# Performance work log

Hardware: AMD Instinct MI355X
Metric: run time of the kernel (lower is better)

The kernel has to match this reference:

```python
import jax, jax.numpy as jnp
import numpy as np

B, T, IN, H, OUT = 64, 512, 512, 1024, 512


def setup_inputs() -> dict:
    key = jax.random.key(0)
    ks = jax.random.split(key, 12)
    s = 0.05
    return {
        "x": jax.random.normal(ks[0], (B, T, IN), dtype=jnp.float32),
        "W_ih0": jax.random.normal(ks[1], (H, IN), dtype=jnp.float32) * s,
        "W_hh0": jax.random.normal(ks[2], (H, H), dtype=jnp.float32) * s,
        "b_ih0": jax.random.normal(ks[3], (H,), dtype=jnp.float32) * s,
        "b_hh0": jax.random.normal(ks[4], (H,), dtype=jnp.float32) * s,
        "W_ih1": jax.random.normal(ks[5], (H, H), dtype=jnp.float32) * s,
        "W_hh1": jax.random.normal(ks[6], (H, H), dtype=jnp.float32) * s,
        "b_ih1": jax.random.normal(ks[7], (H,), dtype=jnp.float32) * s,
        "b_hh1": jax.random.normal(ks[8], (H,), dtype=jnp.float32) * s,
        "fc_w": jax.random.normal(ks[9], (OUT, H), dtype=jnp.float32) * s,
        "fc_b": jax.random.normal(ks[10], (OUT,), dtype=jnp.float32) * s,
    }


def reference(x, W_ih0, W_hh0, b_ih0, b_hh0, W_ih1, W_hh1, b_ih1, b_hh1, fc_w, fc_b):
    # Two-layer Elman RNN with tanh, scanned over time.
    batch = x.shape[0]
    hid = W_hh0.shape[0]
    h_init = jnp.zeros((2, batch, hid), dtype=x.dtype)

    def step(h, x_t):
        h0 = jnp.tanh(x_t @ W_ih0.T + b_ih0 + h[0] @ W_hh0.T + b_hh0)
        h1 = jnp.tanh(h0 @ W_ih1.T + b_ih1 + h[1] @ W_hh1.T + b_hh1)
        return jnp.stack([h0, h1]), h1

    h_final, ys = jax.lax.scan(step, h_init, jnp.swapaxes(x, 0, 1))  # ys: [T,B,H]
    outputs = jnp.swapaxes(ys, 0, 1)  # [B,T,H]
    # Note: the torch module computes fc(outputs[:, -1, :]) but discards it;
    # the returned values are (outputs, h) only.
    return (outputs, h_final)
```

## Files before the change

kernel.cpp:

```cpp
#include <hip/hip_runtime.h>
#include <math.h>

#define RNN_B 64
#define RNN_T 512
#define RNN_IN 512
#define RNN_H 1024


__device__ __forceinline__ void fma16(float4 acc[4], const float4 w, const float4 h) {
  acc[0].x = fmaf(w.x, h.x, acc[0].x); acc[0].y = fmaf(w.x, h.y, acc[0].y);
  acc[0].z = fmaf(w.x, h.z, acc[0].z); acc[0].w = fmaf(w.x, h.w, acc[0].w);
  acc[1].x = fmaf(w.y, h.x, acc[1].x); acc[1].y = fmaf(w.y, h.y, acc[1].y);
  acc[1].z = fmaf(w.y, h.z, acc[1].z); acc[1].w = fmaf(w.y, h.w, acc[1].w);
  acc[2].x = fmaf(w.z, h.x, acc[2].x); acc[2].y = fmaf(w.z, h.y, acc[2].y);
  acc[2].z = fmaf(w.z, h.z, acc[2].z); acc[2].w = fmaf(w.z, h.w, acc[2].w);
  acc[3].x = fmaf(w.w, h.x, acc[3].x); acc[3].y = fmaf(w.w, h.y, acc[3].y);
  acc[3].z = fmaf(w.w, h.z, acc[3].z); acc[3].w = fmaf(w.w, h.w, acc[3].w);
}

__device__ __forceinline__ void reduce4(float4 acc[4]) {
  #pragma unroll
  for (int m = 8; m <= 16; m <<= 1) {
    #pragma unroll
    for (int c = 0; c < 4; ++c) {
      acc[c].x += __shfl_xor(acc[c].x, m, 64);
      acc[c].y += __shfl_xor(acc[c].y, m, 64);
      acc[c].z += __shfl_xor(acc[c].z, m, 64);
      acc[c].w += __shfl_xor(acc[c].w, m, 64);
    }
  }
}

__device__ __forceinline__ void grid_barrier(unsigned* flags, unsigned* gen,
                                             unsigned target) {
  __syncthreads();
  const int tid = threadIdx.x;
  const int bid = blockIdx.x;
  if (tid == 0)
    __hip_atomic_store(flags + bid, target, __ATOMIC_RELAXED,
                       __HIP_MEMORY_SCOPE_AGENT);
  if (bid == 0) {
    if (tid < 64) {
      for (;;) {
        bool ok = true;
        #pragma unroll
        for (int i = 0; i < 4; ++i) {
          unsigned v = __hip_atomic_load(flags + tid + 64 * i, __ATOMIC_RELAXED,
                                         __HIP_MEMORY_SCOPE_AGENT);
          ok &= (v >= target);
        }
        if (__all(ok)) break;
        __builtin_amdgcn_s_sleep(1);
      }
      if (tid < 8)
        __hip_atomic_store(gen + tid * 16, target, __ATOMIC_RELAXED,
                           __HIP_MEMORY_SCOPE_AGENT);
    }
  } else if (tid == 0) {
    while (__hip_atomic_load(gen + (bid & 7) * 16, __ATOMIC_RELAXED,
                             __HIP_MEMORY_SCOPE_AGENT) < target) {
      __builtin_amdgcn_s_sleep(2);
    }
  }
  if (tid == 0)
    __builtin_amdgcn_fence(__ATOMIC_ACQUIRE, "agent");
  __syncthreads();
}

__global__ __launch_bounds__(256) void pre_kernel(
    const float* __restrict__ x, const float* __restrict__ Wih0,
    const float* __restrict__ bih0, const float* __restrict__ bhh0,
    float* __restrict__ out)
{
  __shared__ float xs[64][68];
  __shared__ float wl[64][68];
  const int t  = blockIdx.y;
  const int n0 = blockIdx.x * 64;
  const int tid = threadIdx.x;
  const int tx = tid & 15;
  const int ty = tid >> 4;
  const int kf4 = tid & 15;
  const int row = tid >> 4;

  float4 acc[4];
  acc[0] = acc[1] = acc[2] = acc[3] = make_float4(0.f, 0.f, 0.f, 0.f);

  for (int k0 = 0; k0 < RNN_IN; k0 += 64) {
    #pragma unroll
    for (int r = 0; r < 4; ++r) {
      const int rr = row + 16 * r;
      float4 v = *(const float4*)(x + ((size_t)rr * RNN_T + t) * RNN_IN + k0 + kf4 * 4);
      xs[kf4*4+0][rr] = v.x; xs[kf4*4+1][rr] = v.y;
      xs[kf4*4+2][rr] = v.z; xs[kf4*4+3][rr] = v.w;
      float4 w = *(const float4*)(Wih0 + (size_t)(n0 + rr) * RNN_IN + k0 + kf4 * 4);
      wl[kf4*4+0][rr] = w.x; wl[kf4*4+1][rr] = w.y;
      wl[kf4*4+2][rr] = w.z; wl[kf4*4+3][rr] = w.w;
    }
    __syncthreads();
    #pragma unroll 8
    for (int k = 0; k < 64; ++k) {
      float4 xv = *(const float4*)&xs[k][tx * 4];
      float4 wv = *(const float4*)&wl[k][ty * 4];
      fma16(acc, wv, xv);
    }
    __syncthreads();
  }

  #pragma unroll
  for (int i = 0; i < 4; ++i) {
    const int n = n0 + ty * 4 + i;
    const float bi = bih0[n] + bhh0[n];
    xs[ty*4+i][tx*4+0] = acc[i].x + bi;
    xs[ty*4+i][tx*4+1] = acc[i].y + bi;
    xs[ty*4+i][tx*4+2] = acc[i].z + bi;
    xs[ty*4+i][tx*4+3] = acc[i].w + bi;
  }
  __syncthreads();
  #pragma unroll
  for (int rep = 0; rep < 4; ++rep) {
    const int idx = tid + 256 * rep;
    const int nloc = idx >> 4;
    const int bq4 = idx & 15;
    float4 o = *(const float4*)(&xs[nloc][bq4 * 4]);
    const int gbid = ((n0 + nloc) >> 3) * 2 + (bq4 >> 3);
    const int off  = (nloc & 7) * 32 + (bq4 & 7) * 4;
    const size_t dst = ((size_t)(gbid >> 2) * RNN_T + t) * RNN_H
                     + (size_t)(gbid & 3) * 256 + off;
    *(float4*)(out + dst) = o;
  }
}

__global__ __launch_bounds__(1024) void rnn_kernel(
    const float* __restrict__ Whh0, const float* __restrict__ Wih1,
    const float* __restrict__ Whh1, const float* __restrict__ bih1,
    const float* __restrict__ bhh1, float* __restrict__ out,
    float* __restrict__ hws)
{
  __shared__ float w0[RNN_H * 8];
  __shared__ float w1[RNN_H * 16];
  __shared__ float part0[16 * 256];
  __shared__ float part1[16 * 256];
  __shared__ float tile[256];

  const int tid = threadIdx.x;
  const int bid = blockIdx.x;
  const int n0 = (bid >> 1) * 8;
  const int b0 = (bid & 1) * 32;

  for (int i = tid; i < 8 * RNN_H; i += 1024) {
    const int nl = i >> 10, k = i & 1023;
    w0[k * 8 + nl]             = Whh0[(size_t)(n0 + nl) * RNN_H + k];
    w1[k * 8 + nl]             = Wih1[(size_t)(n0 + nl) * RNN_H + k];
    w1[8 * RNN_H + k * 8 + nl] = Whh1[(size_t)(n0 + nl) * RNN_H + k];
  }
  float mybias = 0.f;
  if (tid < 256) mybias = bih1[n0 + (tid >> 5)] + bhh1[n0 + (tid >> 5)];
  __syncthreads();

  const int wav  = tid >> 6;
  const int lane = tid & 63;
  const int nh   = lane >> 5;
  const int kq   = (lane >> 3) & 3;
  const int bq   = lane & 7;
  const int kbase = wav * 4 + kq;
  const int hoff = kbase * RNN_B + b0 + bq * 4;
  const int woff = kbase * 8 + nh * 4;

  unsigned* flags = (unsigned*)(hws + 262144);
  unsigned* gen   = (unsigned*)(hws + 262400);
  float* h0buf[2] = { hws,         hws + 131072 };
  float* h1buf[2] = { hws + 65536, hws + 196608 };
  const int houtoff = (n0 + (tid >> 5)) * RNN_B + b0 + (tid & 31);

  float preval = 0.f, nextpre = 0.f;
  if (tid < 256)
    preval = out[(size_t)(bid >> 2) * RNN_T * RNN_H + (size_t)(bid & 3) * 256 + tid];

  for (int p = 0; p <= RNN_T; ++p) {
    if (tid < 256 && p + 1 < RNN_T)
      nextpre = out[((size_t)(bid >> 2) * RNN_T + (p + 1)) * RNN_H
                    + (size_t)(bid & 3) * 256 + tid];
    if (p < RNN_T) {
      const float* hp = h0buf[(p + 1) & 1] + hoff;
      const float* wp = w0 + woff;
      float4 acc[4];
      acc[0] = acc[1] = acc[2] = acc[3] = make_float4(0.f, 0.f, 0.f, 0.f);
      #pragma unroll
      for (int j = 0; j < 16; ++j) {
        float4 hv = *(const float4*)(hp + j * 64 * RNN_B);
        float4 wv = *(const float4*)(wp + j * 64 * 8);
        fma16(acc, wv, hv);
      }
      reduce4(acc);
      if ((lane & 24) == 0) {
        #pragma unroll
        for (int c = 0; c < 4; ++c)
          *(float4*)(part0 + wav * 256 + (nh * 4 + c) * 32 + bq * 4) = acc[c];
      }
    }
    if (p >= 1) {
      const int t = p - 1;
      const float* h0t = h0buf[t & 1]       + hoff;
      const float* h1p = h1buf[(t + 1) & 1] + hoff;
      const float* wpa = w1 + woff;
      const float* wpb = w1 + 8 * RNN_H + woff;
      float4 acc[4];
      acc[0] = acc[1] = acc[2] = acc[3] = make_float4(0.f, 0.f, 0.f, 0.f);
      #pragma unroll
      for (int j = 0; j < 16; ++j) {
        float4 hv0 = *(const float4*)(h0t + j * 64 * RNN_B);
        float4 wv0 = *(const float4*)(wpa + j * 64 * 8);
        float4 hv1 = *(const float4*)(h1p + j * 64 * RNN_B);
        float4 wv1 = *(const float4*)(wpb + j * 64 * 8);
        fma16(acc, wv0, hv0);
        fma16(acc, wv1, hv1);
      }
      reduce4(acc);
      if ((lane & 24) == 0) {
        #pragma unroll
        for (int c = 0; c < 4; ++c)
          *(float4*)(part1 + wav * 256 + (nh * 4 + c) * 32 + bq * 4) = acc[c];
      }
    }
    __syncthreads();
    if (tid < 256) {
      if (p < RNN_T) {
        float s = preval;
        #pragma unroll
        for (int w = 0; w < 16; ++w) s += part0[w * 256 + tid];
        __hip_atomic_store(&h0buf[p & 1][houtoff], tanhf(s), __ATOMIC_RELAXED,
                           __HIP_MEMORY_SCOPE_AGENT);
      }
      if (p >= 1) {
        float s = mybias;
        #pragma unroll
        for (int w = 0; w < 16; ++w) s += part1[w * 256 + tid];
        float v = tanhf(s);
        __hip_atomic_store(&h1buf[(p - 1) & 1][houtoff], v, __ATOMIC_RELAXED,
                           __HIP_MEMORY_SCOPE_AGENT);
        tile[tid] = v;
      }
      preval = nextpre;
    }
    __syncthreads();
    if (p >= 1 && tid < 64) {
      const int b = tid >> 1, half = tid & 1;
      float4 o;
      o.x = tile[(half * 4 + 0) * 32 + b];
      o.y = tile[(half * 4 + 1) * 32 + b];
      o.z = tile[(half * 4 + 2) * 32 + b];
      o.w = tile[(half * 4 + 3) * 32 + b];
      *(float4*)(out + ((size_t)(b0 + b) * RNN_T + (p - 1)) * RNN_H + n0 + half * 4) = o;
    }
    if (p < RNN_T) grid_barrier(flags, gen, (unsigned)(p + 1));
  }

  if (tid < 512) {
    const int l   = tid >> 8;
    const int idx = tid & 255;
    const int nl  = idx >> 5, bl = idx & 31;
    const float* hf = (l == 0) ? (hws + 131072) : (hws + 196608);
    float v = __hip_atomic_load(hf + (size_t)(n0 + nl) * RNN_B + b0 + bl,
                                __ATOMIC_RELAXED, __HIP_MEMORY_SCOPE_AGENT);
    out[(size_t)RNN_B * RNN_T * RNN_H + ((size_t)l * RNN_B + b0 + bl) * RNN_H + n0 + nl]
        = v;
  }
}

extern "C" void kernel_launch(void* const* d_in, const int* in_sizes, int n_in,
                              void* d_out, int out_size, void* d_ws, size_t ws_size,
                              hipStream_t stream) {
  (void)in_sizes; (void)n_in; (void)out_size; (void)ws_size;
  const float* x    = (const float*)d_in[0];
  const float* Wih0 = (const float*)d_in[1];
  const float* Whh0 = (const float*)d_in[2];
  const float* bih0 = (const float*)d_in[3];
  const float* bhh0 = (const float*)d_in[4];
  const float* Wih1 = (const float*)d_in[5];
  const float* Whh1 = (const float*)d_in[6];
  const float* bih1 = (const float*)d_in[7];
  const float* bhh1 = (const float*)d_in[8];
  float* out = (float*)d_out;
  float* hws = (float*)d_ws;

  hipMemsetAsync(hws + 131072, 0, (131072 + 256 + 128) * sizeof(float), stream);

  dim3 pg(16, 512);
  pre_kernel<<<pg, 256, 0, stream>>>(x, Wih0, bih0, bhh0, out);

  void* args[] = { (void*)&Whh0, (void*)&Wih1, (void*)&Whh1,
                   (void*)&bih1, (void*)&bhh1, (void*)&out, (void*)&hws };
  hipLaunchCooperativeKernel((const void*)rnn_kernel, dim3(256), dim3(1024),
                             args, 0, stream);
}
```

Measured before the change: 8.591 ms.

## Split grid barrier into arrive/wait, fuse layer matvecs, use fast tanh

Splits the grid barrier into an early arrive and a later wait, so the output-tile store overlaps barrier latency. Fuses the layer-0 and layer-1 matvec loops into one pass that shares the h0 load, and swaps tanhf for an exp2/rcp approximation. Also shortens the spin sleep and adds a minimum-occupancy hint to launch bounds. The fused loop raises register pressure, and the fast tanh may lose accuracy, which then compounds over 512 recurrent steps.

```diff
diff --git a/kernel.cpp b/kernel.cpp
--- a/kernel.cpp
+++ b/kernel.cpp
@@ -31,14 +31,23 @@
   }
 }
 
-__device__ __forceinline__ void grid_barrier(unsigned* flags, unsigned* gen,
+__device__ __forceinline__ float fast_tanh(float x) {
+  float ax = fabsf(x);
+  float z  = __builtin_amdgcn_exp2f(ax * 2.8853900817779268f);
+  float t  = 1.f - 2.f * __builtin_amdgcn_rcpf(z + 1.f);
+  return __builtin_copysignf(t, x);
+}
+
+__device__ __forceinline__ void barrier_arrive(unsigned* flags, unsigned target) {
+  if (threadIdx.x == 0)
+    __hip_atomic_store(flags + blockIdx.x, target, __ATOMIC_RELAXED,
+                       __HIP_MEMORY_SCOPE_AGENT);
+}
+
+__device__ __forceinline__ void barrier_wait(unsigned* flags, unsigned* gen,
                                              unsigned target) {
-  __syncthreads();
   const int tid = threadIdx.x;
   const int bid = blockIdx.x;
-  if (tid == 0)
-    __hip_atomic_store(flags + bid, target, __ATOMIC_RELAXED,
-                       __HIP_MEMORY_SCOPE_AGENT);
   if (bid == 0) {
     if (tid < 64) {
       for (;;) {
@@ -59,7 +68,7 @@
   } else if (tid == 0) {
     while (__hip_atomic_load(gen + (bid & 7) * 16, __ATOMIC_RELAXED,
                              __HIP_MEMORY_SCOPE_AGENT) < target) {
-      __builtin_amdgcn_s_sleep(2);
+      __builtin_amdgcn_s_sleep(1);
     }
   }
   if (tid == 0)
@@ -130,7 +139,7 @@
   }
 }
 
-__global__ __launch_bounds__(1024) void rnn_kernel(
+__global__ __launch_bounds__(1024, 4) void rnn_kernel(
     const float* __restrict__ Whh0, const float* __restrict__ Wih1,
     const float* __restrict__ Whh1, const float* __restrict__ bih1,
     const float* __restrict__ bhh1, float* __restrict__ out,
@@ -180,46 +189,67 @@
     if (tid < 256 && p + 1 < RNN_T)
       nextpre = out[((size_t)(bid >> 2) * RNN_T + (p + 1)) * RNN_H
                     + (size_t)(bid & 3) * 256 + tid];
-    if (p < RNN_T) {
-      const float* hp = h0buf[(p + 1) & 1] + hoff;
-      const float* wp = w0 + woff;
-      float4 acc[4];
-      acc[0] = acc[1] = acc[2] = acc[3] = make_float4(0.f, 0.f, 0.f, 0.f);
+
+    float4 a0[4], a1[4];
+    a0[0] = a0[1] = a0[2] = a0[3] = make_float4(0.f, 0.f, 0.f, 0.f);
+    a1[0] = a1[1] = a1[2] = a1[3] = make_float4(0.f, 0.f, 0.f, 0.f);
+
+    if (p >= 1 && p < RNN_T) {
+      const float* hc  = h0buf[(p + 1) & 1] + hoff;
+      const float* h1p = h1buf[p & 1]       + hoff;
+      const float* wp0 = w0 + woff;
+      const float* wpa = w1 + woff;
+      const float* wpb = w1 + 8 * RNN_H + woff;
       #pragma unroll
       for (int j = 0; j < 16; ++j) {
-        float4 hv = *(const float4*)(hp + j * 64 * RNN_B);
-        float4 wv = *(const float4*)(wp + j * 64 * 8);
-        fma16(acc, wv, hv);
-      }
-      reduce4(acc);
-      if ((lane & 24) == 0) {
-        #pragma unroll
-        for (int c = 0; c < 4; ++c)
-          *(float4*)(part0 + wav * 256 + (nh * 4 + c) * 32 + bq * 4) = acc[c];
-      }
-    }
-    if (p >= 1) {
-      const int t = p - 1;
-      const float* h0t = h0buf[t & 1]       + hoff;
-      const float* h1p = h1buf[(t + 1) & 1] + hoff;
+        float4 h0v = *(const float4*)(hc  + j * 64 * RNN_B);
+        float4 h1v = *(const float4*)(h1p + j * 64 * RNN_B);
+        float4 wv0 = *(const float4*)(wp0 + j * 64 * 8);
+        float4 wva = *(const float4*)(wpa + j * 64 * 8);
+        float4 wvb = *(const float4*)(wpb + j * 64 * 8);
+        fma16(a0, wv0, h0v);
+        fma16(a1, wva, h0v);
+        fma16(a1, wvb, h1v);
+      }
+    } else if (p == 0) {
+      const float* hc  = h0buf[1] + hoff;
+      const float* wp0 = w0 + woff;
+      #pragma unroll
+      for (int j = 0; j < 16; ++j) {
+        float4 h0v = *(const float4*)(hc + j * 64 * RNN_B);
+        float4 wv0 = *(const float4*)(wp0 + j * 64 * 8);
+        fma16(a0, wv0, h0v);
+      }
+    } else {
+      const float* h0t = h0buf[(p + 1) & 1] + hoff;
+      const float* h1p = h1buf[p & 1]       + hoff;
       const float* wpa = w1 + woff;
       const float* wpb = w1 + 8 * RNN_H + woff;
-      float4 acc[4];
-      acc[0] = acc[1] = acc[2] = acc[3] = make_float4(0.f, 0.f, 0.f, 0.f);
       #pragma unroll
       for (int j = 0; j < 16; ++j) {
-        float4 hv0 = *(const float4*)(h0t + j * 64 * RNN_B);
-        float4 wv0 = *(const float4*)(wpa + j * 64 * 8);
-        float4 hv1 = *(const float4*)(h1p + j * 64 * RNN_B);
-        float4 wv1 = *(const float4*)(wpb + j * 64 * 8);
-        fma16(acc, wv0, hv0);
-        fma16(acc, wv1, hv1);
-      }
-      reduce4(acc);
+        float4 h0v = *(const float4*)(h0t + j * 64 * RNN_B);
+        float4 h1v = *(const float4*)(h1p + j * 64 * RNN_B);
+        float4 wva = *(const float4*)(wpa + j * 64 * 8);
+        float4 wvb = *(const float4*)(wpb + j * 64 * 8);
+        fma16(a1, wva, h0v);
+        fma16(a1, wvb, h1v);
+      }
+    }
+
+    if (p < RNN_T) {
+      reduce4(a0);
       if ((lane & 24) == 0) {
         #pragma unroll
         for (int c = 0; c < 4; ++c)
-          *(float4*)(part1 + wav * 256 + (nh * 4 + c) * 32 + bq * 4) = acc[c];
+          *(float4*)(part0 + wav * 256 + (nh * 4 + c) * 32 + bq * 4) = a0[c];
+      }
+    }
+    if (p >= 1) {
+      reduce4(a1);
+      if ((lane & 24) == 0) {
+        #pragma unroll
+        for (int c = 0; c < 4; ++c)
+          *(float4*)(part1 + wav * 256 + (nh * 4 + c) * 32 + bq * 4) = a1[c];
       }
     }
     __syncthreads();
@@ -228,14 +258,14 @@
         float s = preval;
         #pragma unroll
         for (int w = 0; w < 16; ++w) s += part0[w * 256 + tid];
-        __hip_atomic_store(&h0buf[p & 1][houtoff], tanhf(s), __ATOMIC_RELAXED,
+        __hip_atomic_store(&h0buf[p & 1][houtoff], fast_tanh(s), __ATOMIC_RELAXED,
                            __HIP_MEMORY_SCOPE_AGENT);
       }
       if (p >= 1) {
         float s = mybias;
         #pragma unroll
         for (int w = 0; w < 16; ++w) s += part1[w * 256 + tid];
-        float v = tanhf(s);
+        float v = fast_tanh(s);
         __hip_atomic_store(&h1buf[(p - 1) & 1][houtoff], v, __ATOMIC_RELAXED,
                            __HIP_MEMORY_SCOPE_AGENT);
         tile[tid] = v;
@@ -243,6 +273,9 @@
       preval = nextpre;
     }
     __syncthreads();
+
+    if (p < RNN_T) barrier_arrive(flags, (unsigned)(p + 1));
+
     if (p >= 1 && tid < 64) {
       const int b = tid >> 1, half = tid & 1;
       float4 o;
@@ -252,7 +285,8 @@
       o.w = tile[(half * 4 + 3) * 32 + b];
       *(float4*)(out + ((size_t)(b0 + b) * RNN_T + (p - 1)) * RNN_H + n0 + half * 4) = o;
     }
-    if (p < RNN_T) grid_barrier(flags, gen, (unsigned)(p + 1));
+
+    if (p < RNN_T) barrier_wait(flags, gen, (unsigned)(p + 1));
   }
 
   if (tid < 512) {
```

Measured after the change: 8.589 ms. About the same (-0.0%).

## Split grid barrier into per-layer flag waits and use fast tanh

Applied to the files above, without the earlier changes.

The single centralized grid barrier per step is replaced by two flag arrays, one per layer. Each block posts its own progress, and waiters poll all 256 flags directly instead of relaying through block 0. Layer 0's finalize and post now happen before layer 1's matvec, so the two layers' dependencies are synchronized separately and the critical path can shrink. tanhf is also replaced with an exp2/rcp approximation, which is cheaper but slightly less accurate and risks small numerical drift.

```diff
diff --git a/kernel.cpp b/kernel.cpp
--- a/kernel.cpp
+++ b/kernel.cpp
@@ -31,40 +31,37 @@
   }
 }
 
-__device__ __forceinline__ void grid_barrier(unsigned* flags, unsigned* gen,
-                                             unsigned target) {
-  __syncthreads();
+__device__ __forceinline__ float fast_tanh(float x) {
+  float ax = fabsf(x);
+  float z  = __builtin_amdgcn_exp2f(ax * 2.8853900817779268f);
+  float t  = 1.f - 2.f * __builtin_amdgcn_rcpf(z + 1.f);
+  return __builtin_copysignf(t, x);
+}
+
+__device__ __forceinline__ void wait_ge(unsigned* arr, int target, bool fence) {
   const int tid = threadIdx.x;
-  const int bid = blockIdx.x;
-  if (tid == 0)
-    __hip_atomic_store(flags + bid, target, __ATOMIC_RELAXED,
-                       __HIP_MEMORY_SCOPE_AGENT);
-  if (bid == 0) {
-    if (tid < 64) {
-      for (;;) {
-        bool ok = true;
-        #pragma unroll
-        for (int i = 0; i < 4; ++i) {
-          unsigned v = __hip_atomic_load(flags + tid + 64 * i, __ATOMIC_RELAXED,
-                                         __HIP_MEMORY_SCOPE_AGENT);
-          ok &= (v >= target);
-        }
-        if (__all(ok)) break;
-        __builtin_amdgcn_s_sleep(1);
-      }
-      if (tid < 8)
-        __hip_atomic_store(gen + tid * 16, target, __ATOMIC_RELAXED,
-                           __HIP_MEMORY_SCOPE_AGENT);
-    }
-  } else if (tid == 0) {
-    while (__hip_atomic_load(gen + (bid & 7) * 16, __ATOMIC_RELAXED,
-                             __HIP_MEMORY_SCOPE_AGENT) < target) {
-      __builtin_amdgcn_s_sleep(2);
-    }
-  }
-  if (tid == 0)
+  if (tid < 64 && target > 0) {
+    for (;;) {
+      bool ok = true;
+      #pragma unroll
+      for (int i = 0; i < 4; ++i) {
+        unsigned v = __hip_atomic_load(arr + tid + 64 * i, __ATOMIC_RELAXED,
+                                       __HIP_MEMORY_SCOPE_AGENT);
+        ok &= ((int)v >= target);
+      }
+      if (__all(ok)) break;
+      __builtin_amdgcn_s_sleep(1);
+    }
+  }
+  if (fence && tid == 0)
     __builtin_amdgcn_fence(__ATOMIC_ACQUIRE, "agent");
   __syncthreads();
+}
+
+__device__ __forceinline__ void post(unsigned* arr, unsigned v) {
+  if (threadIdx.x == 0)
+    __hip_atomic_store(arr + blockIdx.x, v, __ATOMIC_RELAXED,
+                       __HIP_MEMORY_SCOPE_AGENT);
 }
 
 __global__ __launch_bounds__(256) void pre_kernel(
@@ -160,14 +157,14 @@
   const int wav  = tid >> 6;
   const int lane = tid & 63;
   const int nh   = lane >> 5;
+  const int bq   = lane & 7;
   const int kq   = (lane >> 3) & 3;
-  const int bq   = lane & 7;
   const int kbase = wav * 4 + kq;
   const int hoff = kbase * RNN_B + b0 + bq * 4;
   const int woff = kbase * 8 + nh * 4;
 
-  unsigned* flags = (unsigned*)(hws + 262144);
-  unsigned* gen   = (unsigned*)(hws + 262400);
+  unsigned* f0 = (unsigned*)(hws + 262144);
+  unsigned* f1 = (unsigned*)(hws + 262400);
   float* h0buf[2] = { hws,         hws + 131072 };
   float* h1buf[2] = { hws + 65536, hws + 196608 };
   const int houtoff = (n0 + (tid >> 5)) * RNN_B + b0 + (tid & 31);
@@ -177,9 +174,11 @@
     preval = out[(size_t)(bid >> 2) * RNN_T * RNN_H + (size_t)(bid & 3) * 256 + tid];
 
   for (int p = 0; p <= RNN_T; ++p) {
+    wait_ge(f0, p, true);
     if (tid < 256 && p + 1 < RNN_T)
       nextpre = out[((size_t)(bid >> 2) * RNN_T + (p + 1)) * RNN_H
                     + (size_t)(bid & 3) * 256 + tid];
+
     if (p < RNN_T) {
       const float* hp = h0buf[(p + 1) & 1] + hoff;
       const float* wp = w0 + woff;
@@ -198,6 +197,21 @@
           *(float4*)(part0 + wav * 256 + (nh * 4 + c) * 32 + bq * 4) = acc[c];
       }
     }
+
+    wait_ge(f1, p, false);
+
+    if (p < RNN_T && tid < 256) {
+      float s = preval;
+      #pragma unroll
+      for (int w = 0; w < 16; ++w) s += part0[w * 256 + tid];
+      __hip_atomic_store(&h0buf[p & 1][houtoff], fast_tanh(s), __ATOMIC_RELAXED,
+                         __HIP_MEMORY_SCOPE_AGENT);
+    }
+    if (tid < 256) preval = nextpre;
+    __syncthreads();
+    if (p < RNN_T) post(f0, (unsigned)(p + 1));
+    if (p == 0)   post(f1, 1u);
+
     if (p >= 1) {
       const int t = p - 1;
       const float* h0t = h0buf[t & 1]       + hoff;
@@ -221,38 +235,28 @@
         for (int c = 0; c < 4; ++c)
           *(float4*)(part1 + wav * 256 + (nh * 4 + c) * 32 + bq * 4) = acc[c];
       }
-    }
-    __syncthreads();
-    if (tid < 256) {
-      if (p < RNN_T) {
-        float s = preval;
-        #pragma unroll
-        for (int w = 0; w < 16; ++w) s += part0[w * 256 + tid];
-        __hip_atomic_store(&h0buf[p & 1][houtoff], tanhf(s), __ATOMIC_RELAXED,
-                           __HIP_MEMORY_SCOPE_AGENT);
-      }
-      if (p >= 1) {
+      __syncthreads();
+      if (tid < 256) {
         float s = mybias;
         #pragma unroll
         for (int w = 0; w < 16; ++w) s += part1[w * 256 + tid];
-        float v = tanhf(s);
-        __hip_atomic_store(&h1buf[(p - 1) & 1][houtoff], v, __ATOMIC_RELAXED,
+        float v = fast_tanh(s);
+        __hip_atomic_store(&h1buf[t & 1][houtoff], v, __ATOMIC_RELAXED,
                            __HIP_MEMORY_SCOPE_AGENT);
         tile[tid] = v;
       }
-      preval = nextpre;
-    }
-    __syncthreads();
-    if (p >= 1 && tid < 64) {
-      const int b = tid >> 1, half = tid & 1;
-      float4 o;
-      o.x = tile[(half * 4 + 0) * 32 + b];
-      o.y = tile[(half * 4 + 1) * 32 + b];
-      o.z = tile[(half * 4 + 2) * 32 + b];
-      o.w = tile[(half * 4 + 3) * 32 + b];
-      *(float4*)(out + ((size_t)(b0 + b) * RNN_T + (p - 1)) * RNN_H + n0 + half * 4) = o;
-    }
-    if (p < RNN_T) grid_barrier(flags, gen, (unsigned)(p + 1));
+      __syncthreads();
+      post(f1, (unsigned)(p + 1));
+      if (tid < 64) {
+        const int b = tid >> 1, half = tid & 1;
+        float4 o;
+        o.x = tile[(half * 4 + 0) * 32 + b];
+        o.y = tile[(half * 4 + 1) * 32 + b];
+        o.z = tile[(half * 4 + 2) * 32 + b];
+        o.w = tile[(half * 4 + 3) * 32 + b];
+        *(float4*)(out + ((size_t)(b0 + b) * RNN_T + t) * RNN_H + n0 + half * 4) = o;
+      }
+    }
   }
 
   if (tid < 512) {
@@ -283,7 +287,7 @@
   float* out = (float*)d_out;
   float* hws = (float*)d_ws;
 
-  hipMemsetAsync(hws + 131072, 0, (131072 + 256 + 128) * sizeof(float), stream);
+  hipMemsetAsync(hws + 131072, 0, (131072 + 512) * sizeof(float), stream);
 
   dim3 pg(16, 512);
   pre_kernel<<<pg, 256, 0, stream>>>(x, Wih0, bih0, bhh0, out);
```

Measured after the change: 7.905 ms. -8.0%, faster.
